# Kernel optimization log

Measured on AMD Instinct MI355X. Metric: run time of the kernel, lower is better.

The kernel has to match this reference:

```python
import jax, jax.numpy as jnp
import numpy as np
from jax import lax

EPS = 1e-10

def _safe_norm(x):
    # torch remove_zeros: replace exact-zero norms with 1e-10
    n = jnp.linalg.norm(x, axis=-1, keepdims=True)
    return jnp.where(n != 0, n, jnp.full_like(n, EPS))

def setup_inputs() -> dict:
    key = jax.random.key(0)
    ks = jax.random.split(key, 5)
    S, B, D = 2048, 32, 512  # seq, batch, 2*hidden
    K = 147  # odd(max_entries/14)
    return {
        "encoder_outputs": jax.random.normal(ks[0], (S, B, D), dtype=jnp.float32),
        "state": jax.random.normal(ks[1], (B, D), dtype=jnp.float32),
        "previous_attention": jax.random.uniform(ks[2], (B, S), dtype=jnp.float32),
        "W_att": jax.random.normal(ks[3], (D, D), dtype=jnp.float32) / np.sqrt(D),
        "b_att": jax.random.normal(ks[4], (D,), dtype=jnp.float32) * 0.01,
        "conv_w": jnp.ones((1, 1, K), dtype=jnp.float32),
        "conv_b": jnp.zeros((1,), dtype=jnp.float32),
    }

def reference(encoder_outputs, state, previous_attention, W_att, b_att, conv_w, conv_b):
    S, B, D = encoder_outputs.shape
    # attended state via linear layer, then cosine-similarity weights (vectorized over seq)
    attended = state @ W_att.T + b_att                       # [B, D]
    ns = attended / _safe_norm(attended)                     # [B, D]
    ne = encoder_outputs / _safe_norm(encoder_outputs)       # [S, B, D]
    weights = jnp.einsum('bd,sbd->bs', ns, ne)               # [B, S]
    # conv1d time smoothing of previous attention (same-length, odd kernel)
    k = conv_w.shape[-1]
    pad = k // 2
    y = lax.conv_general_dilated(previous_attention[:, None, :], conv_w,
                                 window_strides=(1,), padding=[(pad, pad)])
    adjusted = jax.nn.relu(y[:, 0, :] + conv_b)              # [B, S]
    prev_probs = adjusted / jnp.sum(adjusted, axis=1, keepdims=True)
    adj = prev_probs * jax.nn.softmax(weights, axis=1)
    norm_w = adj / jnp.sum(adj, axis=1, keepdims=True)       # [B, S]
    applied = jnp.einsum('bs,sbd->bd', norm_w, encoder_outputs)  # [B, D]
    return applied, norm_w
```

## Files before the change

kernel.cpp:

```cpp
#include <hip/hip_runtime.h>
#include <math.h>


__device__ __forceinline__ float wave_sum(float v) {
    for (int off = 32; off; off >>= 1) v += __shfl_xor(v, off);
    return v;
}

__global__ __launch_bounds__(256) void front_kernel(
    const float* __restrict__ state, const float* __restrict__ W,
    const float* __restrict__ bias, const float* __restrict__ prev,
    const float* __restrict__ cw, const float* __restrict__ cb,
    float* __restrict__ ns, float* __restrict__ adj,
    int S, int D, int K) {
    __shared__ __align__(16) float smem[1024];
    __shared__ float red[4];
    int b = blockIdx.y;
    int t = threadIdx.x;
    int lane = t & 63, wv = t >> 6;

    if (blockIdx.x == 0) {
        if (t < D / 4)
            ((float4*)smem)[t] = ((const float4*)(state + (size_t)b * D))[t];
        __syncthreads();
        const float4* sv = (const float4*)smem;
        float acc0 = bias[t];
        float acc1 = bias[t + 256];
        const float4* W0 = (const float4*)(W + (size_t)t * D);
        const float4* W1 = (const float4*)(W + (size_t)(t + 256) * D);
#pragma unroll 8
        for (int k = 0; k < 128; ++k) {
            float4 s4 = sv[k];
            float4 w0 = W0[k];
            float4 w1 = W1[k];
            acc0 += w0.x * s4.x + w0.y * s4.y + w0.z * s4.z + w0.w * s4.w;
            acc1 += w1.x * s4.x + w1.y * s4.y + w1.z * s4.z + w1.w * s4.w;
        }
        float sq = acc0 * acc0 + acc1 * acc1;
        sq = wave_sum(sq);
        if (lane == 0) red[wv] = sq;
        __syncthreads();
        float tot = red[0] + red[1] + red[2] + red[3];
        float inv = (tot > 0.f) ? __builtin_amdgcn_rsqf(tot) : 0.f;
        ns[(size_t)b * D + t] = acc0 * inv;
        ns[(size_t)b * D + t + 256] = acc1 * inv;
    } else {
        int s0 = (blockIdx.x - 1) * 256;
        int pad = K / 2;
        int seglen = 256 + K - 1;
        float* seg = smem;
        float* wk = smem + 512;
        for (int i = t; i < seglen; i += 256) {
            int s = s0 - pad + i;
            seg[i] = (s >= 0 && s < S) ? prev[(size_t)b * S + s] : 0.f;
        }
        for (int j = t; j < K; j += 256) wk[j] = cw[j];
        __syncthreads();
        float y = cb[0];
        for (int j = 0; j < K; ++j) y += seg[t + j] * wk[j];
        adj[(size_t)b * S + s0 + t] = fmaxf(y, 0.f);
    }
}

__global__ __launch_bounds__(256) void main_kernel(
    const float* __restrict__ e, const float* __restrict__ ns,
    const float* __restrict__ adj, float* __restrict__ partial,
    float* __restrict__ zbuf, float* __restrict__ u,
    int S, int B, int D) {
    constexpr int CH = 8;
    int wave = threadIdx.x >> 6;
    int lane = threadIdx.x & 63;
    int b = blockIdx.y * 4 + wave;
    int sx = blockIdx.x;
    int s0 = sx * CH;

    const float4* ns4 = (const float4*)(ns + (size_t)b * D);
    float4 ns0 = ns4[lane];
    float4 ns1 = ns4[lane + 64];

    float adjv = (lane < CH) ? adj[(size_t)b * S + s0 + lane] : 0.f;

    float4 acc0 = {0.f, 0.f, 0.f, 0.f};
    float4 acc1 = {0.f, 0.f, 0.f, 0.f};
    float z = 0.f;

    const float4* row4 = (const float4*)(e + ((size_t)s0 * B + b) * D);
    size_t rstride = (size_t)B * D / 4;

#pragma unroll 2
    for (int i = 0; i < CH; i += 2) {
        float4 xa0 = row4[lane];
        float4 xa1 = row4[lane + 64];
        float4 xb0 = row4[rstride + lane];
        float4 xb1 = row4[rstride + lane + 64];
        float ava = __shfl(adjv, i);
        float avb = __shfl(adjv, i + 1);
        float dota = xa0.x * ns0.x + xa0.y * ns0.y + xa0.z * ns0.z + xa0.w * ns0.w
                   + xa1.x * ns1.x + xa1.y * ns1.y + xa1.z * ns1.z + xa1.w * ns1.w;
        float sqa  = xa0.x * xa0.x + xa0.y * xa0.y + xa0.z * xa0.z + xa0.w * xa0.w
                   + xa1.x * xa1.x + xa1.y * xa1.y + xa1.z * xa1.z + xa1.w * xa1.w;
        float dotb = xb0.x * ns0.x + xb0.y * ns0.y + xb0.z * ns0.z + xb0.w * ns0.w
                   + xb1.x * ns1.x + xb1.y * ns1.y + xb1.z * ns1.z + xb1.w * ns1.w;
        float sqb  = xb0.x * xb0.x + xb0.y * xb0.y + xb0.z * xb0.z + xb0.w * xb0.w
                   + xb1.x * xb1.x + xb1.y * xb1.y + xb1.z * xb1.z + xb1.w * xb1.w;
#pragma unroll
        for (int off = 32; off; off >>= 1) {
            dota += __shfl_xor(dota, off);
            dotb += __shfl_xor(dotb, off);
            sqa  += __shfl_xor(sqa, off);
            sqb  += __shfl_xor(sqb, off);
        }
        float ra = (sqa > 0.f) ? __builtin_amdgcn_rsqf(sqa) : 0.f;
        float rb = (sqb > 0.f) ? __builtin_amdgcn_rsqf(sqb) : 0.f;
        float coefa = ava * __expf(dota * ra);
        float coefb = avb * __expf(dotb * rb);
        if (lane == 0)
            *((float2*)(u + (size_t)b * S + s0 + i)) = make_float2(coefa, coefb);
        acc0.x += coefa * xa0.x + coefb * xb0.x;
        acc0.y += coefa * xa0.y + coefb * xb0.y;
        acc0.z += coefa * xa0.z + coefb * xb0.z;
        acc0.w += coefa * xa0.w + coefb * xb0.w;
        acc1.x += coefa * xa1.x + coefb * xb1.x;
        acc1.y += coefa * xa1.y + coefb * xb1.y;
        acc1.z += coefa * xa1.z + coefb * xb1.z;
        acc1.w += coefa * xa1.w + coefb * xb1.w;
        z += coefa + coefb;
        row4 += 2 * rstride;
    }

    float4* p4 = (float4*)(partial + ((size_t)sx * B + b) * D);
    p4[lane] = acc0;
    p4[lane + 64] = acc1;
    if (lane == 0) zbuf[(size_t)sx * B + b] = z;
}

__global__ __launch_bounds__(256) void combine_kernel(
    const float* __restrict__ partial, const float* __restrict__ zbuf,
    const float* __restrict__ u, float* __restrict__ applied,
    float* __restrict__ norm_w, int S, int B, int D, int NPART) {
    int q = blockIdx.x;
    int b = blockIdx.y;
    int t = threadIdx.x;
    __shared__ __align__(16) float4 red4[8][32];
    __shared__ float zred[4];
    __shared__ float zsh;

    float zt = (t < NPART) ? zbuf[(size_t)t * B + b] : 0.f;
    zt = wave_sum(zt);
    if ((t & 63) == 0) zred[t >> 6] = zt;

    int c2 = t >> 5;
    int di = t & 31;
    int d4 = q * 32 + di;
    const float4* p4 = (const float4*)partial;
    float4 a = {0.f, 0.f, 0.f, 0.f};
    for (int cix = c2; cix < NPART; cix += 8) {
        float4 x = p4[((size_t)cix * B + b) * (D >> 2) + d4];
        a.x += x.x; a.y += x.y; a.z += x.z; a.w += x.w;
    }
    red4[c2][di] = a;
    __syncthreads();
    if (t == 0) zsh = 1.f / (zred[0] + zred[1] + zred[2] + zred[3]);
    __syncthreads();
    float inv = zsh;
    if (t < 32) {
        float4 s = red4[0][t];
#pragma unroll
        for (int j = 1; j < 8; ++j) {
            float4 x = red4[j][t];
            s.x += x.x; s.y += x.y; s.z += x.z; s.w += x.w;
        }
        s.x *= inv; s.y *= inv; s.z *= inv; s.w *= inv;
        ((float4*)(applied + (size_t)b * D))[q * 32 + t] = s;
    }

    const float4* u4 = (const float4*)(u + (size_t)b * S);
    float4* nw4 = (float4*)(norm_w + (size_t)b * S);
    if (t < 128) {
        int idx = q * (S >> 4) + t;
        float4 x = u4[idx];
        x.x *= inv; x.y *= inv; x.z *= inv; x.w *= inv;
        nw4[idx] = x;
    }
}

extern "C" void kernel_launch(void* const* d_in, const int* in_sizes, int n_in,
                              void* d_out, int out_size, void* d_ws, size_t ws_size,
                              hipStream_t stream) {
    const float* enc   = (const float*)d_in[0];
    const float* state = (const float*)d_in[1];
    const float* prev  = (const float*)d_in[2];
    const float* W     = (const float*)d_in[3];
    const float* bias  = (const float*)d_in[4];
    const float* cw    = (const float*)d_in[5];
    const float* cb    = (const float*)d_in[6];

    const int S = in_sizes[0] / in_sizes[1];
    const int B = in_sizes[2] / S;
    const int D = in_sizes[1] / B;
    const int K = in_sizes[5];

    float* out     = (float*)d_out;
    float* applied = out;
    float* norm_w  = out + (size_t)B * D;

    const int CH = 8;
    const int NPART = S / CH;

    float* ws       = (float*)d_ws;
    float* nsbuf    = ws;
    float* adj      = nsbuf + (size_t)B * D;
    float* u        = adj + (size_t)B * S;
    float* zbuf     = u + (size_t)B * S;
    float* partial  = zbuf + (size_t)NPART * B;

    front_kernel<<<dim3(1 + S / 256, B), 256, 0, stream>>>(
        state, W, bias, prev, cw, cb, nsbuf, adj, S, D, K);
    main_kernel<<<dim3(S / CH, B / 4), 256, 0, stream>>>(
        enc, nsbuf, adj, partial, zbuf, u, S, B, D);
    combine_kernel<<<dim3(4, B), 256, 0, stream>>>(
        partial, zbuf, u, applied, norm_w, S, B, D, NPART);
}
```

Baseline: 250.1 us.

## Double-buffer four-row encoder loads and double the rows per partial block

Result: slower. 276.0 us (+10.4%).

```diff
diff --git a/kernel.cpp b/kernel.cpp
--- a/kernel.cpp
+++ b/kernel.cpp
@@ -62,17 +62,67 @@
     }
 }
 
-__global__ __launch_bounds__(256) void main_kernel(
+#define LOADG(Xa0, Xb0, Xa1, Xb1, Xa2, Xb2, Xa3, Xb3, base)                  \
+    Xa0 = (base)[lane];                Xb0 = (base)[lane + 64];              \
+    Xa1 = (base)[rstride + lane];      Xb1 = (base)[rstride + lane + 64];    \
+    Xa2 = (base)[2 * rstride + lane];  Xb2 = (base)[2 * rstride + lane + 64];\
+    Xa3 = (base)[3 * rstride + lane];  Xb3 = (base)[3 * rstride + lane + 64];
+
+#define DOTSQ(d, q, Xa, Xb)                                                  \
+    d = Xa.x * ns0.x + Xa.y * ns0.y + Xa.z * ns0.z + Xa.w * ns0.w            \
+      + Xb.x * ns1.x + Xb.y * ns1.y + Xb.z * ns1.z + Xb.w * ns1.w;           \
+    q = Xa.x * Xa.x + Xa.y * Xa.y + Xa.z * Xa.z + Xa.w * Xa.w                \
+      + Xb.x * Xb.x + Xb.y * Xb.y + Xb.z * Xb.z + Xb.w * Xb.w;
+
+#define PROC(gi, Xa0, Xb0, Xa1, Xb1, Xa2, Xb2, Xa3, Xb3)                     \
+    {                                                                        \
+        float d0, d1, d2, d3, q0, q1, q2, q3;                                \
+        DOTSQ(d0, q0, Xa0, Xb0)                                              \
+        DOTSQ(d1, q1, Xa1, Xb1)                                              \
+        DOTSQ(d2, q2, Xa2, Xb2)                                              \
+        DOTSQ(d3, q3, Xa3, Xb3)                                              \
+        _Pragma("unroll")                                                    \
+        for (int off = 32; off; off >>= 1) {                                 \
+            d0 += __shfl_xor(d0, off); d1 += __shfl_xor(d1, off);            \
+            d2 += __shfl_xor(d2, off); d3 += __shfl_xor(d3, off);            \
+            q0 += __shfl_xor(q0, off); q1 += __shfl_xor(q1, off);            \
+            q2 += __shfl_xor(q2, off); q3 += __shfl_xor(q3, off);            \
+        }                                                                    \
+        float r0 = (q0 > 0.f) ? __builtin_amdgcn_rsqf(q0) : 0.f;             \
+        float r1 = (q1 > 0.f) ? __builtin_amdgcn_rsqf(q1) : 0.f;             \
+        float r2 = (q2 > 0.f) ? __builtin_amdgcn_rsqf(q2) : 0.f;             \
+        float r3 = (q3 > 0.f) ? __builtin_amdgcn_rsqf(q3) : 0.f;             \
+        float c0 = __shfl(adjv, (gi))     * __expf(d0 * r0);                 \
+        float c1 = __shfl(adjv, (gi) + 1) * __expf(d1 * r1);                 \
+        float c2 = __shfl(adjv, (gi) + 2) * __expf(d2 * r2);                 \
+        float c3 = __shfl(adjv, (gi) + 3) * __expf(d3 * r3);                 \
+        if (lane == 0) {                                                     \
+            float4 cv = {c0, c1, c2, c3};                                    \
+            *((float4*)(u + (size_t)b * S + s0 + (gi))) = cv;                \
+        }                                                                    \
+        acc0.x += c0 * Xa0.x + c1 * Xa1.x + c2 * Xa2.x + c3 * Xa3.x;         \
+        acc0.y += c0 * Xa0.y + c1 * Xa1.y + c2 * Xa2.y + c3 * Xa3.y;         \
+        acc0.z += c0 * Xa0.z + c1 * Xa1.z + c2 * Xa2.z + c3 * Xa3.z;         \
+        acc0.w += c0 * Xa0.w + c1 * Xa1.w + c2 * Xa2.w + c3 * Xa3.w;         \
+        acc1.x += c0 * Xb0.x + c1 * Xb1.x + c2 * Xb2.x + c3 * Xb3.x;         \
+        acc1.y += c0 * Xb0.y + c1 * Xb1.y + c2 * Xb2.y + c3 * Xb3.y;         \
+        acc1.z += c0 * Xb0.z + c1 * Xb1.z + c2 * Xb2.z + c3 * Xb3.z;         \
+        acc1.w += c0 * Xb0.w + c1 * Xb1.w + c2 * Xb2.w + c3 * Xb3.w;         \
+        z += (c0 + c1) + (c2 + c3);                                          \
+    }
+
+__global__ __launch_bounds__(256, 4) void main_kernel(
     const float* __restrict__ e, const float* __restrict__ ns,
     const float* __restrict__ adj, float* __restrict__ partial,
     float* __restrict__ zbuf, float* __restrict__ u,
     int S, int B, int D) {
-    constexpr int CH = 8;
+    constexpr int CH = 16;
     int wave = threadIdx.x >> 6;
     int lane = threadIdx.x & 63;
     int b = blockIdx.y * 4 + wave;
     int sx = blockIdx.x;
     int s0 = sx * CH;
+    int NPART = gridDim.x;
 
     const float4* ns4 = (const float4*)(ns + (size_t)b * D);
     float4 ns0 = ns4[lane];
@@ -87,51 +137,22 @@
     const float4* row4 = (const float4*)(e + ((size_t)s0 * B + b) * D);
     size_t rstride = (size_t)B * D / 4;
 
-#pragma unroll 2
-    for (int i = 0; i < CH; i += 2) {
-        float4 xa0 = row4[lane];
-        float4 xa1 = row4[lane + 64];
-        float4 xb0 = row4[rstride + lane];
-        float4 xb1 = row4[rstride + lane + 64];
-        float ava = __shfl(adjv, i);
-        float avb = __shfl(adjv, i + 1);
-        float dota = xa0.x * ns0.x + xa0.y * ns0.y + xa0.z * ns0.z + xa0.w * ns0.w
-                   + xa1.x * ns1.x + xa1.y * ns1.y + xa1.z * ns1.z + xa1.w * ns1.w;
-        float sqa  = xa0.x * xa0.x + xa0.y * xa0.y + xa0.z * xa0.z + xa0.w * xa0.w
-                   + xa1.x * xa1.x + xa1.y * xa1.y + xa1.z * xa1.z + xa1.w * xa1.w;
-        float dotb = xb0.x * ns0.x + xb0.y * ns0.y + xb0.z * ns0.z + xb0.w * ns0.w
-                   + xb1.x * ns1.x + xb1.y * ns1.y + xb1.z * ns1.z + xb1.w * ns1.w;
-        float sqb  = xb0.x * xb0.x + xb0.y * xb0.y + xb0.z * xb0.z + xb0.w * xb0.w
-                   + xb1.x * xb1.x + xb1.y * xb1.y + xb1.z * xb1.z + xb1.w * xb1.w;
-#pragma unroll
-        for (int off = 32; off; off >>= 1) {
-            dota += __shfl_xor(dota, off);
-            dotb += __shfl_xor(dotb, off);
-            sqa  += __shfl_xor(sqa, off);
-            sqb  += __shfl_xor(sqb, off);
-        }
-        float ra = (sqa > 0.f) ? __builtin_amdgcn_rsqf(sqa) : 0.f;
-        float rb = (sqb > 0.f) ? __builtin_amdgcn_rsqf(sqb) : 0.f;
-        float coefa = ava * __expf(dota * ra);
-        float coefb = avb * __expf(dotb * rb);
-        if (lane == 0)
-            *((float2*)(u + (size_t)b * S + s0 + i)) = make_float2(coefa, coefb);
-        acc0.x += coefa * xa0.x + coefb * xb0.x;
-        acc0.y += coefa * xa0.y + coefb * xb0.y;
-        acc0.z += coefa * xa0.z + coefb * xb0.z;
-        acc0.w += coefa * xa0.w + coefb * xb0.w;
-        acc1.x += coefa * xa1.x + coefb * xb1.x;
-        acc1.y += coefa * xa1.y + coefb * xb1.y;
-        acc1.z += coefa * xa1.z + coefb * xb1.z;
-        acc1.w += coefa * xa1.w + coefb * xb1.w;
-        z += coefa + coefb;
-        row4 += 2 * rstride;
-    }
-
-    float4* p4 = (float4*)(partial + ((size_t)sx * B + b) * D);
+    float4 Aa0, Ab0, Aa1, Ab1, Aa2, Ab2, Aa3, Ab3;
+    float4 Ba0, Bb0, Ba1, Bb1, Ba2, Bb2, Ba3, Bb3;
+
+    LOADG(Aa0, Ab0, Aa1, Ab1, Aa2, Ab2, Aa3, Ab3, row4)
+    LOADG(Ba0, Bb0, Ba1, Bb1, Ba2, Bb2, Ba3, Bb3, row4 + 4 * rstride)
+    PROC(0, Aa0, Ab0, Aa1, Ab1, Aa2, Ab2, Aa3, Ab3)
+    LOADG(Aa0, Ab0, Aa1, Ab1, Aa2, Ab2, Aa3, Ab3, row4 + 8 * rstride)
+    PROC(4, Ba0, Bb0, Ba1, Bb1, Ba2, Bb2, Ba3, Bb3)
+    LOADG(Ba0, Bb0, Ba1, Bb1, Ba2, Bb2, Ba3, Bb3, row4 + 12 * rstride)
+    PROC(8, Aa0, Ab0, Aa1, Ab1, Aa2, Ab2, Aa3, Ab3)
+    PROC(12, Ba0, Bb0, Ba1, Bb1, Ba2, Bb2, Ba3, Bb3)
+
+    float4* p4 = (float4*)(partial + ((size_t)b * NPART + sx) * D);
     p4[lane] = acc0;
     p4[lane + 64] = acc1;
-    if (lane == 0) zbuf[(size_t)sx * B + b] = z;
+    if (lane == 0) zbuf[(size_t)b * NPART + sx] = z;
 }
 
 __global__ __launch_bounds__(256) void combine_kernel(
@@ -145,7 +166,7 @@
     __shared__ float zred[4];
     __shared__ float zsh;
 
-    float zt = (t < NPART) ? zbuf[(size_t)t * B + b] : 0.f;
+    float zt = (t < NPART) ? zbuf[(size_t)b * NPART + t] : 0.f;
     zt = wave_sum(zt);
     if ((t & 63) == 0) zred[t >> 6] = zt;
 
@@ -154,8 +175,8 @@
     int d4 = q * 32 + di;
     const float4* p4 = (const float4*)partial;
     float4 a = {0.f, 0.f, 0.f, 0.f};
-    for (int cix = c2; cix < NPART; cix += 8) {
-        float4 x = p4[((size_t)cix * B + b) * (D >> 2) + d4];
+    for (int sx = c2; sx < NPART; sx += 8) {
+        float4 x = p4[((size_t)b * NPART + sx) * (D >> 2) + d4];
         a.x += x.x; a.y += x.y; a.z += x.z; a.w += x.w;
     }
     red4[c2][di] = a;
@@ -204,7 +225,7 @@
     float* applied = out;
     float* norm_w  = out + (size_t)B * D;
 
-    const int CH = 8;
+    const int CH = 16;
     const int NPART = S / CH;
 
     float* ws       = (float*)d_ws;
@@ -212,7 +233,7 @@
     float* adj      = nsbuf + (size_t)B * D;
     float* u        = adj + (size_t)B * S;
     float* zbuf     = u + (size_t)B * S;
-    float* partial  = zbuf + (size_t)NPART * B;
+    float* partial  = zbuf + (size_t)B * NPART;
 
     front_kernel<<<dim3(1 + S / 256, B), 256, 0, stream>>>(
         state, W, bias, prev, cw, cb, nsbuf, adj, S, D, K);
```

## Pipeline encoder loads through LDS with async global_load_lds triple buffering

Applied to the files above, without the earlier changes.

Measured after the change: 250.9 us. About the same (+0.3%).

```diff
diff --git a/kernel.cpp b/kernel.cpp
--- a/kernel.cpp
+++ b/kernel.cpp
@@ -5,6 +5,12 @@
 __device__ __forceinline__ float wave_sum(float v) {
     for (int off = 32; off; off >>= 1) v += __shfl_xor(v, off);
     return v;
+}
+
+__device__ __forceinline__ void gll16(const float4* g, float4* l) {
+    __builtin_amdgcn_global_load_lds(
+        (const __attribute__((address_space(1))) void*)g,
+        (__attribute__((address_space(3))) void*)l, 16, 0, 0);
 }
 
 __global__ __launch_bounds__(256) void front_kernel(
@@ -62,76 +68,108 @@
     }
 }
 
+#define STAGE(buf, g)                                                        \
+    {                                                                        \
+        const float4* gs = row4 + (size_t)(2 * (g)) * rstride;               \
+        float4* ld = (float4*)&lds4[wave][(buf)][0];                         \
+        gll16(gs + lane, ld);                                                \
+        gll16(gs + lane + 64, ld + 64);                                      \
+        gll16(gs + rstride + lane, ld + 128);                                \
+        gll16(gs + rstride + lane + 64, ld + 192);                           \
+    }
+
+#define WAITV(n) asm volatile("s_waitcnt vmcnt(" #n ")" ::: "memory")
+
+#define COMPUTE(buf, g, C0, C1)                                              \
+    {                                                                        \
+        const float4* ld = (const float4*)&lds4[wave][(buf)][0];             \
+        float4 xa0 = ld[lane];                                               \
+        float4 xa1 = ld[lane + 64];                                          \
+        float4 xb0 = ld[lane + 128];                                         \
+        float4 xb1 = ld[lane + 192];                                         \
+        float dota = xa0.x * ns0.x + xa0.y * ns0.y + xa0.z * ns0.z           \
+                   + xa0.w * ns0.w + xa1.x * ns1.x + xa1.y * ns1.y           \
+                   + xa1.z * ns1.z + xa1.w * ns1.w;                          \
+        float sqa  = xa0.x * xa0.x + xa0.y * xa0.y + xa0.z * xa0.z           \
+                   + xa0.w * xa0.w + xa1.x * xa1.x + xa1.y * xa1.y           \
+                   + xa1.z * xa1.z + xa1.w * xa1.w;                          \
+        float dotb = xb0.x * ns0.x + xb0.y * ns0.y + xb0.z * ns0.z           \
+                   + xb0.w * ns0.w + xb1.x * ns1.x + xb1.y * ns1.y           \
+                   + xb1.z * ns1.z + xb1.w * ns1.w;                          \
+        float sqb  = xb0.x * xb0.x + xb0.y * xb0.y + xb0.z * xb0.z           \
+                   + xb0.w * xb0.w + xb1.x * xb1.x + xb1.y * xb1.y           \
+                   + xb1.z * xb1.z + xb1.w * xb1.w;                          \
+        _Pragma("unroll")                                                    \
+        for (int off = 32; off; off >>= 1) {                                 \
+            dota += __shfl_xor(dota, off);                                   \
+            dotb += __shfl_xor(dotb, off);                                   \
+            sqa  += __shfl_xor(sqa, off);                                    \
+            sqb  += __shfl_xor(sqb, off);                                    \
+        }                                                                    \
+        float ra = (sqa > 0.f) ? __builtin_amdgcn_rsqf(sqa) : 0.f;           \
+        float rb = (sqb > 0.f) ? __builtin_amdgcn_rsqf(sqb) : 0.f;           \
+        float c0 = __shfl(adjv, 2 * (g)) * __expf(dota * ra);                \
+        float c1 = __shfl(adjv, 2 * (g) + 1) * __expf(dotb * rb);            \
+        C0 = c0;                                                             \
+        C1 = c1;                                                             \
+        acc0.x += c0 * xa0.x + c1 * xb0.x;                                   \
+        acc0.y += c0 * xa0.y + c1 * xb0.y;                                   \
+        acc0.z += c0 * xa0.z + c1 * xb0.z;                                   \
+        acc0.w += c0 * xa0.w + c1 * xb0.w;                                   \
+        acc1.x += c0 * xa1.x + c1 * xb1.x;                                   \
+        acc1.y += c0 * xa1.y + c1 * xb1.y;                                   \
+        acc1.z += c0 * xa1.z + c1 * xb1.z;                                   \
+        acc1.w += c0 * xa1.w + c1 * xb1.w;                                   \
+        z += c0 + c1;                                                        \
+    }
+
 __global__ __launch_bounds__(256) void main_kernel(
     const float* __restrict__ e, const float* __restrict__ ns,
     const float* __restrict__ adj, float* __restrict__ partial,
     float* __restrict__ zbuf, float* __restrict__ u,
     int S, int B, int D) {
-    constexpr int CH = 8;
+    constexpr int CH = 16;
+    __shared__ __align__(16) float4 lds4[4][3][256];
     int wave = threadIdx.x >> 6;
     int lane = threadIdx.x & 63;
-    int b = blockIdx.y * 4 + wave;
-    int sx = blockIdx.x;
-    int s0 = sx * CH;
+    int c = blockIdx.x * 4 + wave;
+    int b = blockIdx.y;
+    int NCH = gridDim.x * 4;
+    int s0 = c * CH;
 
     const float4* ns4 = (const float4*)(ns + (size_t)b * D);
     float4 ns0 = ns4[lane];
     float4 ns1 = ns4[lane + 64];
-
     float adjv = (lane < CH) ? adj[(size_t)b * S + s0 + lane] : 0.f;
 
     float4 acc0 = {0.f, 0.f, 0.f, 0.f};
     float4 acc1 = {0.f, 0.f, 0.f, 0.f};
     float z = 0.f;
+    float4 up0, up1, up2, up3;
 
     const float4* row4 = (const float4*)(e + ((size_t)s0 * B + b) * D);
     size_t rstride = (size_t)B * D / 4;
 
-#pragma unroll 2
-    for (int i = 0; i < CH; i += 2) {
-        float4 xa0 = row4[lane];
-        float4 xa1 = row4[lane + 64];
-        float4 xb0 = row4[rstride + lane];
-        float4 xb1 = row4[rstride + lane + 64];
-        float ava = __shfl(adjv, i);
-        float avb = __shfl(adjv, i + 1);
-        float dota = xa0.x * ns0.x + xa0.y * ns0.y + xa0.z * ns0.z + xa0.w * ns0.w
-                   + xa1.x * ns1.x + xa1.y * ns1.y + xa1.z * ns1.z + xa1.w * ns1.w;
-        float sqa  = xa0.x * xa0.x + xa0.y * xa0.y + xa0.z * xa0.z + xa0.w * xa0.w
-                   + xa1.x * xa1.x + xa1.y * xa1.y + xa1.z * xa1.z + xa1.w * xa1.w;
-        float dotb = xb0.x * ns0.x + xb0.y * ns0.y + xb0.z * ns0.z + xb0.w * ns0.w
-                   + xb1.x * ns1.x + xb1.y * ns1.y + xb1.z * ns1.z + xb1.w * ns1.w;
-        float sqb  = xb0.x * xb0.x + xb0.y * xb0.y + xb0.z * xb0.z + xb0.w * xb0.w
-                   + xb1.x * xb1.x + xb1.y * xb1.y + xb1.z * xb1.z + xb1.w * xb1.w;
-#pragma unroll
-        for (int off = 32; off; off >>= 1) {
-            dota += __shfl_xor(dota, off);
-            dotb += __shfl_xor(dotb, off);
-            sqa  += __shfl_xor(sqa, off);
-            sqb  += __shfl_xor(sqb, off);
-        }
-        float ra = (sqa > 0.f) ? __builtin_amdgcn_rsqf(sqa) : 0.f;
-        float rb = (sqb > 0.f) ? __builtin_amdgcn_rsqf(sqb) : 0.f;
-        float coefa = ava * __expf(dota * ra);
-        float coefb = avb * __expf(dotb * rb);
-        if (lane == 0)
-            *((float2*)(u + (size_t)b * S + s0 + i)) = make_float2(coefa, coefb);
-        acc0.x += coefa * xa0.x + coefb * xb0.x;
-        acc0.y += coefa * xa0.y + coefb * xb0.y;
-        acc0.z += coefa * xa0.z + coefb * xb0.z;
-        acc0.w += coefa * xa0.w + coefb * xb0.w;
-        acc1.x += coefa * xa1.x + coefb * xb1.x;
-        acc1.y += coefa * xa1.y + coefb * xb1.y;
-        acc1.z += coefa * xa1.z + coefb * xb1.z;
-        acc1.w += coefa * xa1.w + coefb * xb1.w;
-        z += coefa + coefb;
-        row4 += 2 * rstride;
-    }
-
-    float4* p4 = (float4*)(partial + ((size_t)sx * B + b) * D);
+    STAGE(0, 0)
+    STAGE(1, 1)
+    STAGE(2, 2)
+    WAITV(8); COMPUTE(0, 0, up0.x, up0.y) STAGE(0, 3)
+    WAITV(8); COMPUTE(1, 1, up0.z, up0.w) STAGE(1, 4)
+    WAITV(8); COMPUTE(2, 2, up1.x, up1.y) STAGE(2, 5)
+    WAITV(8); COMPUTE(0, 3, up1.z, up1.w) STAGE(0, 6)
+    WAITV(8); COMPUTE(1, 4, up2.x, up2.y) STAGE(1, 7)
+    WAITV(8); COMPUTE(2, 5, up2.z, up2.w)
+    WAITV(4); COMPUTE(0, 6, up3.x, up3.y)
+    WAITV(0); COMPUTE(1, 7, up3.z, up3.w)
+
+    if (lane == 0) {
+        float4* up = (float4*)(u + (size_t)b * S + s0);
+        up[0] = up0; up[1] = up1; up[2] = up2; up[3] = up3;
+        zbuf[(size_t)b * NCH + c] = z;
+    }
+    float4* p4 = (float4*)(partial + ((size_t)b * NCH + c) * D);
     p4[lane] = acc0;
     p4[lane + 64] = acc1;
-    if (lane == 0) zbuf[(size_t)sx * B + b] = z;
 }
 
 __global__ __launch_bounds__(256) void combine_kernel(
@@ -145,7 +183,7 @@
     __shared__ float zred[4];
     __shared__ float zsh;
 
-    float zt = (t < NPART) ? zbuf[(size_t)t * B + b] : 0.f;
+    float zt = (t < NPART) ? zbuf[(size_t)b * NPART + t] : 0.f;
     zt = wave_sum(zt);
     if ((t & 63) == 0) zred[t >> 6] = zt;
 
@@ -155,7 +193,7 @@
     const float4* p4 = (const float4*)partial;
     float4 a = {0.f, 0.f, 0.f, 0.f};
     for (int cix = c2; cix < NPART; cix += 8) {
-        float4 x = p4[((size_t)cix * B + b) * (D >> 2) + d4];
+        float4 x = p4[((size_t)b * NPART + cix) * (D >> 2) + d4];
         a.x += x.x; a.y += x.y; a.z += x.z; a.w += x.w;
     }
     red4[c2][di] = a;
@@ -204,7 +242,7 @@
     float* applied = out;
     float* norm_w  = out + (size_t)B * D;
 
-    const int CH = 8;
+    const int CH = 16;
     const int NPART = S / CH;
 
     float* ws       = (float*)d_ws;
@@ -212,11 +250,11 @@
     float* adj      = nsbuf + (size_t)B * D;
     float* u        = adj + (size_t)B * S;
     float* zbuf     = u + (size_t)B * S;
-    float* partial  = zbuf + (size_t)NPART * B;
+    float* partial  = zbuf + (size_t)B * NPART;
 
     front_kernel<<<dim3(1 + S / 256, B), 256, 0, stream>>>(
         state, W, bias, prev, cw, cb, nsbuf, adj, S, D, K);
-    main_kernel<<<dim3(S / CH, B / 4), 256, 0, stream>>>(
+    main_kernel<<<dim3(NPART / 4, B), 256, 0, stream>>>(
         enc, nsbuf, adj, partial, zbuf, u, S, B, D);
     combine_kernel<<<dim3(4, B), 256, 0, stream>>>(
         partial, zbuf, u, applied, norm_w, S, B, D, NPART);
```
